# Performance work log

Hardware: AMD Instinct MI355X
Metric: run time of the kernel (lower is better)

## Reference

```python
import jax, jax.numpy as jnp
import numpy as np

B, S, D, H = 4, 2048, 1024, 16
DK = D // H

def setup_inputs() -> dict:
    key = jax.random.key(0)
    ks = jax.random.split(key, 11)
    scale = 1.0 / np.sqrt(D)
    return {
        "query": jax.random.normal(ks[0], (B, S, D), jnp.float32),
        "key_": jax.random.normal(ks[1], (B, S, D), jnp.float32),
        "value": jax.random.normal(ks[2], (B, S, D), jnp.float32),
        "Wq": jax.random.normal(ks[3], (D, D), jnp.float32) * scale,
        "bq": jnp.zeros((D,), jnp.float32),
        "Wk": jax.random.normal(ks[4], (D, D), jnp.float32) * scale,
        "bk": jnp.zeros((D,), jnp.float32),
        "Wv": jax.random.normal(ks[5], (D, D), jnp.float32) * scale,
        "bv": jnp.zeros((D,), jnp.float32),
        "Wo": jax.random.normal(ks[6], (D, D), jnp.float32) * scale,
        "bo": jnp.zeros((D,), jnp.float32),
    }

def reference(query, key_, value, Wq, bq, Wk, bk, Wv, bv, Wo, bo):
    # Linear projections (torch Linear: x @ W.T + b)
    Q = query @ Wq.T + bq            # [B,S,D]
    K = key_ @ Wk.T + bk
    V = value @ Wv.T + bv
    # split heads -> [B,H,S,DK]
    def split(x):
        return x.reshape(B, S, H, DK).transpose(0, 2, 1, 3)
    Qh, Kh, Vh = split(Q), split(K), split(V)
    scores = jnp.einsum("bhqd,bhkd->bhqk", Qh, Kh) / np.sqrt(DK)
    attn = jax.nn.softmax(scores, axis=-1)
    ctx = jnp.einsum("bhqk,bhkd->bhqd", attn, Vh)
    ctx = ctx.transpose(0, 2, 1, 3).reshape(B, S, D)
    return ctx @ Wo.T + bo
```

## Files before the change

### kernel.cpp

```cpp
#include <hip/hip_runtime.h>
#include <hip/hip_bf16.h>
#include <stdint.h>

#define B_ 4
#define S_ 2048
#define D_ 1024
#define H_ 16
#define DK_ 64
#define GM (B_ * S_)
#define GN D_
#define GK D_
#define BM 128
#define BN 128
#define BK 64
#define QBLK 128
#define KVBLK 128

typedef __attribute__((ext_vector_type(8))) __bf16 bf16x8;
typedef __attribute__((ext_vector_type(4))) float f32x4;
typedef __attribute__((ext_vector_type(4))) uint32_t u32x4;
typedef __attribute__((ext_vector_type(2))) uint32_t u32x2;

#if __has_builtin(__builtin_amdgcn_exp2f)
#define EXP2F(x) __builtin_amdgcn_exp2f(x)
#else
#define EXP2F(x) exp2f(x)
#endif

#define SCALE_LOG2E 0.18033688011112042f

__device__ __forceinline__ uint16_t f2bf(float x) {
  uint32_t u = __builtin_bit_cast(uint32_t, x);
  u += 0x7fffu + ((u >> 16) & 1u);
  return (uint16_t)(u >> 16);
}
__device__ __forceinline__ uint32_t cvtpk(float lo, float hi) {
  uint32_t r;
  asm("v_cvt_pk_bf16_f32 %0, %1, %2" : "=v"(r) : "v"(lo), "v"(hi));
  return r;
}
__device__ __forceinline__ void gload_lds16(const void* g, void* l) {
  __builtin_amdgcn_global_load_lds(
      (const __attribute__((address_space(1))) void*)g,
      (__attribute__((address_space(3))) void*)l, 16, 0, 0);
}

struct CvtArgs {
  const float* src[7];
  uint16_t* dst[7];
  int n[7];
  float scale[7];
};

__global__ __launch_bounds__(256) void cvt_f32_bf16(CvtArgs a) {
  const int z = blockIdx.z;
  const float* __restrict__ s = a.src[z];
  uint16_t* __restrict__ d = a.dst[z];
  const float sc = a.scale[z];
  const int nv = a.n[z] >> 3;
  const int stride = gridDim.x * blockDim.x;
  for (int i = blockIdx.x * blockDim.x + threadIdx.x; i < nv; i += stride) {
    f32x4 v0 = *(const f32x4*)(s + (size_t)i * 8);
    f32x4 v1 = *(const f32x4*)(s + (size_t)i * 8 + 4);
    union { uint16_t u[8]; u32x4 q; } o;
#pragma unroll
    for (int j = 0; j < 4; ++j) o.u[j] = f2bf(v0[j] * sc);
#pragma unroll
    for (int j = 0; j < 4; ++j) o.u[4 + j] = f2bf(v1[j] * sc);
    *(u32x4*)(d + (size_t)i * 8) = o.q;
  }
}

struct Gemm3Args {
  const uint16_t* A[3];
  const uint16_t* W[3];
  const float* bias[3];
  float bscale[3];
  void* C[3];
};

template <bool CF32>
__global__ __launch_bounds__(256, 2) void mha_gemm3(Gemm3Args args) {
  const int z = blockIdx.z;
  const char* __restrict__ A = (const char*)args.A[z];
  const char* __restrict__ W = (const char*)args.W[z];
  const float* __restrict__ bias = args.bias[z];
  const float bsc = args.bscale[z];
  void* __restrict__ C = args.C[z];

  __shared__ alignas(16) uint16_t tA[BM][BK];
  __shared__ alignas(16) uint16_t tW[BN][BK];

  const int tid = threadIdx.x;
  const int lane = tid & 63;
  const int wid = tid >> 6;
  const int wm = wid >> 1, wn = wid & 1;
  const int l16 = lane & 15, g = lane >> 4;

  const int m0 = blockIdx.y * BM;
  const int n0 = blockIdx.x * BN;

  f32x4 acc[4][4] = {};
  const int o = tid * 16;

  for (int k0 = 0; k0 < GK; k0 += BK) {
#pragma unroll
    for (int i = 0; i < 4; ++i) {
      const int oo = o + i * 4096;
      const int row = oo >> 7, colb = oo & 127;
      gload_lds16(A + (size_t)(m0 + row) * (GK * 2) + (size_t)k0 * 2 + colb,
                  ((char*)&tA[0][0]) + i * 4096 + wid * 1024);
      gload_lds16(W + (size_t)(n0 + row) * (GK * 2) + (size_t)k0 * 2 + colb,
                  ((char*)&tW[0][0]) + i * 4096 + wid * 1024);
    }
    __syncthreads();
#pragma unroll
    for (int kk = 0; kk < 2; ++kk) {
      const int kcol = kk * 32 + g * 8;
      bf16x8 af[4], bfr[4];
#pragma unroll
      for (int m = 0; m < 4; ++m)
        af[m] = *(const bf16x8*)&tA[wm * 64 + m * 16 + l16][kcol];
#pragma unroll
      for (int n = 0; n < 4; ++n)
        bfr[n] = *(const bf16x8*)&tW[wn * 64 + n * 16 + l16][kcol];
#pragma unroll
      for (int m = 0; m < 4; ++m)
#pragma unroll
        for (int n = 0; n < 4; ++n)
          acc[m][n] = __builtin_amdgcn_mfma_f32_16x16x32_bf16(
              af[m], bfr[n], acc[m][n], 0, 0, 0);
    }
    __syncthreads();
  }

#pragma unroll
  for (int n = 0; n < 4; ++n) {
    const int col = n0 + wn * 64 + n * 16 + l16;
    const float bv = bias[col] * bsc;
#pragma unroll
    for (int m = 0; m < 4; ++m) {
      const int rbase = m0 + wm * 64 + m * 16 + g * 4;
#pragma unroll
      for (int r = 0; r < 4; ++r) {
        const float v = acc[m][n][r] + bv;
        if (CF32)
          ((float*)C)[(size_t)(rbase + r) * GN + col] = v;
        else
          ((uint16_t*)C)[(size_t)(rbase + r) * GN + col] = f2bf(v);
      }
    }
  }
}

__global__ __launch_bounds__(256) void transpose_v(
    const uint16_t* __restrict__ Vp, uint16_t* __restrict__ Vt) {
  __shared__ alignas(16) char T[64 * 128];
  const int tid = threadIdx.x;
  const int s0 = blockIdx.x * 64;
  const int h = blockIdx.y;
  const int bb = blockIdx.z;
#pragma unroll
  for (int it = 0; it < 2; ++it) {
    const int idx = tid + it * 256;
    const int row = idx >> 3;
    const int colb = (idx & 7) * 16;
    const u32x4 v = *(const u32x4*)((const char*)Vp +
        (((size_t)bb * S_ + s0 + row) * D_ + h * DK_) * 2 + colb);
    *(u32x4*)(T + row * 128 + (colb ^ (((row >> 3) & 7) << 4))) = v;
  }
  __syncthreads();
#pragma unroll
  for (int it = 0; it < 2; ++it) {
    const int idx = tid + it * 256;
    const int dk = idx >> 3;
    const int sc = (idx & 7) * 8;
    union { uint16_t u[8]; u32x4 q; } o;
#pragma unroll
    for (int j = 0; j < 8; ++j) {
      const int row = sc + j;
      o.u[j] =
          *(const uint16_t*)(T + row * 128 + ((dk * 2) ^ (((row >> 3) & 7) << 4)));
    }
    *(u32x4*)((char*)Vt +
              (((size_t)(bb * H_ + h) * DK_ + dk) * S_ + s0 + sc) * 2) = o.q;
  }
}

__global__ __launch_bounds__(256) void mha_attn(
    const uint16_t* __restrict__ Q, const uint16_t* __restrict__ K,
    const uint16_t* __restrict__ Vt, uint16_t* __restrict__ O) {
  __shared__ alignas(16) char K_s[2][16384];
  __shared__ alignas(16) char V_s[2][16384];

  const int tid = threadIdx.x;
  const int lane = tid & 63;
  const int wid = tid >> 6;
  const int l16 = lane & 15, g = lane >> 4;

  const int d = blockIdx.x;
  const int bh = (d & 7) + ((d >> 7) << 3);
  const int qb = (d >> 3) & 15;
  const int b = bh >> 4, h = bh & 15;
  const int q0 = qb * QBLK;

  bf16x8 qf[2][2];
#pragma unroll
  for (int mi = 0; mi < 2; ++mi) {
    const uint16_t* qp = Q + ((size_t)(b * S_) + q0 + mi * 64 + wid * 16 + l16) * D_ +
                         h * DK_ + g * 8;
    qf[mi][0] = *(const bf16x8*)qp;
    qf[mi][1] = *(const bf16x8*)(qp + 32);
  }

  f32x4 o_acc[2][4] = {};
  float lpart[2] = {0.f, 0.f};

  const char* Kb = (const char*)K;
  const char* Vtb = (const char*)Vt;

  int srowK[4], scolK[4], srowV[4], scolV[4];
#pragma unroll
  for (int i = 0; i < 4; ++i) {
    const int oo = tid * 16 + i * 4096;
    srowK[i] = oo >> 7;
    scolK[i] = (oo & 127) ^ ((srowK[i] & 7) << 4);
    srowV[i] = oo >> 8;
    scolV[i] = (oo & 255) ^ ((srowV[i] & 7) << 4);
  }

#define ISSUE_LOADS(buf, kv0)                                                  \
  {                                                                            \
    _Pragma("unroll") for (int i = 0; i < 4; ++i) {                            \
      gload_lds16(Kb + (((size_t)b * S_ + (kv0) + srowK[i]) * D_ + h * DK_) * 2\
                      + scolK[i],                                              \
                  &K_s[buf][0] + i * 4096 + wid * 1024);                       \
      gload_lds16(Vtb + (((size_t)bh * DK_ + srowV[i]) * S_ + (kv0)) * 2       \
                      + scolV[i],                                              \
                  &V_s[buf][0] + i * 4096 + wid * 1024);                       \
    }                                                                          \
  }

  ISSUE_LOADS(0, 0);
  __syncthreads();
  int cur = 0;

  const int bsrc = l16 + ((g & 1) << 5);
  const int gsel = g >> 1;

  for (int kv0 = 0; kv0 < S_; kv0 += KVBLK) {
    const bool last = (kv0 + KVBLK >= S_);
    if (!last) ISSUE_LOADS(cur ^ 1, kv0 + KVBLK);

    f32x4 sacc[2][8] = {};
#pragma unroll
    for (int ks = 0; ks < 2; ++ks) {
      const int kcolb = ks * 64 + g * 16;
#pragma unroll
      for (int n = 0; n < 8; ++n) {
        const int kvr = n * 16 + l16;
        const bf16x8 kf =
            *(const bf16x8*)(&K_s[cur][0] + kvr * 128 + (kcolb ^ ((kvr & 7) << 4)));
#pragma unroll
        for (int mi = 0; mi < 2; ++mi)
          sacc[mi][n] = __builtin_amdgcn_mfma_f32_16x16x32_bf16(
              kf, qf[mi][ks], sacc[mi][n], 0, 0, 0);
      }
    }

    uint32_t pb[2][4][4];
#pragma unroll
    for (int mi = 0; mi < 2; ++mi) {
      uint32_t pk0[8][2];
#pragma unroll
      for (int n = 0; n < 8; ++n) {
        float e0 = EXP2F(sacc[mi][n][0]);
        float e1 = EXP2F(sacc[mi][n][1]);
        float e2 = EXP2F(sacc[mi][n][2]);
        float e3 = EXP2F(sacc[mi][n][3]);
        lpart[mi] += (e0 + e1) + (e2 + e3);
        pk0[n][0] = cvtpk(e0, e1);
        pk0[n][1] = cvtpk(e2, e3);
      }
#pragma unroll
      for (int ks = 0; ks < 4; ++ks)
#pragma unroll
        for (int jp = 0; jp < 4; ++jp) {
          const int srcl = bsrc + ((jp >> 1) << 4);
          const uint32_t va = __shfl(pk0[2 * ks][jp & 1], srcl, 64);
          const uint32_t vb = __shfl(pk0[2 * ks + 1][jp & 1], srcl, 64);
          pb[mi][ks][jp] = gsel ? vb : va;
        }
    }

#pragma unroll
    for (int ks = 0; ks < 4; ++ks) {
      const int kcolb = ks * 64 + g * 16;
      bf16x8 pf[2];
#pragma unroll
      for (int mi = 0; mi < 2; ++mi) {
        u32x4 t = {pb[mi][ks][0], pb[mi][ks][1], pb[mi][ks][2], pb[mi][ks][3]};
        pf[mi] = __builtin_bit_cast(bf16x8, t);
      }
#pragma unroll
      for (int n = 0; n < 4; ++n) {
        const int dkr = n * 16 + l16;
        const bf16x8 vf =
            *(const bf16x8*)(&V_s[cur][0] + dkr * 256 + (kcolb ^ ((dkr & 7) << 4)));
#pragma unroll
        for (int mi = 0; mi < 2; ++mi)
          o_acc[mi][n] = __builtin_amdgcn_mfma_f32_16x16x32_bf16(
              vf, pf[mi], o_acc[mi][n], 0, 0, 0);
      }
    }

    if (!last) __syncthreads();
    cur ^= 1;
  }

  float linv[2];
#pragma unroll
  for (int mi = 0; mi < 2; ++mi) {
    float s_ = lpart[mi];
    s_ += __shfl_xor(s_, 16, 64);
    s_ += __shfl_xor(s_, 32, 64);
    linv[mi] = 1.f / s_;
  }
#pragma unroll
  for (int mi = 0; mi < 2; ++mi) {
    const size_t row = (size_t)b * S_ + q0 + mi * 64 + wid * 16 + l16;
    uint16_t* op = O + row * D_ + h * DK_ + g * 4;
#pragma unroll
    for (int n = 0; n < 4; ++n) {
      u32x2 w;
      w[0] = cvtpk(o_acc[mi][n][0] * linv[mi], o_acc[mi][n][1] * linv[mi]);
      w[1] = cvtpk(o_acc[mi][n][2] * linv[mi], o_acc[mi][n][3] * linv[mi]);
      *(u32x2*)(op + n * 16) = w;
    }
  }
}

extern "C" void kernel_launch(void* const* d_in, const int* in_sizes, int n_in,
                              void* d_out, int out_size, void* d_ws,
                              size_t ws_size, hipStream_t stream) {
  (void)in_sizes; (void)n_in; (void)out_size; (void)ws_size;

  const float* query = (const float*)d_in[0];
  const float* key_ = (const float*)d_in[1];
  const float* value = (const float*)d_in[2];
  const float* Wq = (const float*)d_in[3];
  const float* bq = (const float*)d_in[4];
  const float* Wk = (const float*)d_in[5];
  const float* bk = (const float*)d_in[6];
  const float* Wv = (const float*)d_in[7];
  const float* bv = (const float*)d_in[8];
  const float* Wo = (const float*)d_in[9];
  const float* bo = (const float*)d_in[10];

  const size_t nact = (size_t)GM * GN;
  const size_t nw = (size_t)GN * GK;
  uint16_t* p = (uint16_t*)d_ws;
  uint16_t* qb = p; p += nact;
  uint16_t* kb = p; p += nact;
  uint16_t* vb = p; p += nact;
  uint16_t* wq = p; p += nw;
  uint16_t* wk = p; p += nw;
  uint16_t* wv = p; p += nw;
  uint16_t* wo = p; p += nw;
  uint16_t* Qp = p; p += nact;
  uint16_t* Kp = p; p += nact;
  uint16_t* Vp = p; p += nact;
  uint16_t* Cp = p; p += nact;
  uint16_t* Vt = qb;

  CvtArgs ca;
  const float* srcs[7] = {query, key_, value, Wq, Wk, Wv, Wo};
  uint16_t* dsts[7] = {qb, kb, vb, wq, wk, wv, wo};
  const int cnts[7] = {(int)nact, (int)nact, (int)nact, (int)nw,
                       (int)nw,   (int)nw,   (int)nw};
  for (int i = 0; i < 7; ++i) {
    ca.src[i] = srcs[i]; ca.dst[i] = dsts[i]; ca.n[i] = cnts[i];
    ca.scale[i] = 1.0f;
  }
  ca.scale[3] = SCALE_LOG2E;
  cvt_f32_bf16<<<dim3(512, 1, 7), dim3(256), 0, stream>>>(ca);

  Gemm3Args g1;
  g1.A[0] = qb; g1.A[1] = kb; g1.A[2] = vb;
  g1.W[0] = wq; g1.W[1] = wk; g1.W[2] = wv;
  g1.bias[0] = bq; g1.bias[1] = bk; g1.bias[2] = bv;
  g1.bscale[0] = SCALE_LOG2E; g1.bscale[1] = 1.0f; g1.bscale[2] = 1.0f;
  g1.C[0] = Qp; g1.C[1] = Kp; g1.C[2] = Vp;
  mha_gemm3<false>
      <<<dim3(GN / BN, GM / BM, 3), dim3(256), 0, stream>>>(g1);

  transpose_v<<<dim3(S_ / 64, H_, B_), dim3(256), 0, stream>>>(Vp, Vt);

  mha_attn<<<dim3((S_ / QBLK) * B_ * H_), dim3(256), 0, stream>>>(Qp, Kp, Vt, Cp);

  Gemm3Args g2;
  g2.A[0] = Cp; g2.W[0] = wo; g2.bias[0] = bo; g2.C[0] = d_out;
  g2.bscale[0] = 1.0f;
  g2.A[1] = g2.A[0]; g2.W[1] = g2.W[0]; g2.bias[1] = g2.bias[0]; g2.C[1] = g2.C[0];
  g2.bscale[1] = 1.0f;
  g2.A[2] = g2.A[0]; g2.W[2] = g2.W[0]; g2.bias[2] = g2.bias[0]; g2.C[2] = g2.C[0];
  g2.bscale[2] = 1.0f;
  mha_gemm3<true>
      <<<dim3(GN / BN, GM / BM, 1), dim3(256), 0, stream>>>(g2);
}
```

Before: 253.0 us.

## Compute V projection transposed directly, removing separate transpose kernel

The V projection is now computed as Wv @ value^T through a separate GEMM launch with a row-broadcast bias and a custom output leading dimension. This writes V already in [h*dk][b*S] layout, so the transpose_v kernel and its extra read and write of V are gone. The attention kernel's V load addressing is updated to the new layout. The fused QKV launch shrinks to two z-slices and a separate V GEMM launch is added. The transposed output stores may coalesce less well than before.

```diff
diff --git a/kernel.cpp b/kernel.cpp
--- a/kernel.cpp
+++ b/kernel.cpp
@@ -15,6 +15,7 @@
 #define BK 64
 #define QBLK 128
 #define KVBLK 128
+#define LDV 8192
 
 typedef __attribute__((ext_vector_type(8))) __bf16 bf16x8;
 typedef __attribute__((ext_vector_type(4))) float f32x4;
@@ -77,9 +78,10 @@
   const float* bias[3];
   float bscale[3];
   void* C[3];
+  int ldc[3];
 };
 
-template <bool CF32>
+template <bool CF32, bool BROW>
 __global__ __launch_bounds__(256, 2) void mha_gemm3(Gemm3Args args) {
   const int z = blockIdx.z;
   const char* __restrict__ A = (const char*)args.A[z];
@@ -87,6 +89,7 @@
   const float* __restrict__ bias = args.bias[z];
   const float bsc = args.bscale[z];
   void* __restrict__ C = args.C[z];
+  const int ldc = args.ldc[z];
 
   __shared__ alignas(16) uint16_t tA[BM][BK];
   __shared__ alignas(16) uint16_t tW[BN][BK];
@@ -137,53 +140,20 @@
 #pragma unroll
   for (int n = 0; n < 4; ++n) {
     const int col = n0 + wn * 64 + n * 16 + l16;
-    const float bv = bias[col] * bsc;
+    const float bvc = BROW ? 0.f : bias[col] * bsc;
 #pragma unroll
     for (int m = 0; m < 4; ++m) {
       const int rbase = m0 + wm * 64 + m * 16 + g * 4;
 #pragma unroll
       for (int r = 0; r < 4; ++r) {
+        const float bv = BROW ? bias[rbase + r] * bsc : bvc;
         const float v = acc[m][n][r] + bv;
         if (CF32)
-          ((float*)C)[(size_t)(rbase + r) * GN + col] = v;
+          ((float*)C)[(size_t)(rbase + r) * ldc + col] = v;
         else
-          ((uint16_t*)C)[(size_t)(rbase + r) * GN + col] = f2bf(v);
-      }
-    }
-  }
-}
-
-__global__ __launch_bounds__(256) void transpose_v(
-    const uint16_t* __restrict__ Vp, uint16_t* __restrict__ Vt) {
-  __shared__ alignas(16) char T[64 * 128];
-  const int tid = threadIdx.x;
-  const int s0 = blockIdx.x * 64;
-  const int h = blockIdx.y;
-  const int bb = blockIdx.z;
-#pragma unroll
-  for (int it = 0; it < 2; ++it) {
-    const int idx = tid + it * 256;
-    const int row = idx >> 3;
-    const int colb = (idx & 7) * 16;
-    const u32x4 v = *(const u32x4*)((const char*)Vp +
-        (((size_t)bb * S_ + s0 + row) * D_ + h * DK_) * 2 + colb);
-    *(u32x4*)(T + row * 128 + (colb ^ (((row >> 3) & 7) << 4))) = v;
-  }
-  __syncthreads();
-#pragma unroll
-  for (int it = 0; it < 2; ++it) {
-    const int idx = tid + it * 256;
-    const int dk = idx >> 3;
-    const int sc = (idx & 7) * 8;
-    union { uint16_t u[8]; u32x4 q; } o;
-#pragma unroll
-    for (int j = 0; j < 8; ++j) {
-      const int row = sc + j;
-      o.u[j] =
-          *(const uint16_t*)(T + row * 128 + ((dk * 2) ^ (((row >> 3) & 7) << 4)));
-    }
-    *(u32x4*)((char*)Vt +
-              (((size_t)(bb * H_ + h) * DK_ + dk) * S_ + s0 + sc) * 2) = o.q;
+          ((uint16_t*)C)[(size_t)(rbase + r) * ldc + col] = f2bf(v);
+      }
+    }
   }
 }
 
@@ -235,8 +205,8 @@
       gload_lds16(Kb + (((size_t)b * S_ + (kv0) + srowK[i]) * D_ + h * DK_) * 2\
                       + scolK[i],                                              \
                   &K_s[buf][0] + i * 4096 + wid * 1024);                       \
-      gload_lds16(Vtb + (((size_t)bh * DK_ + srowV[i]) * S_ + (kv0)) * 2       \
-                      + scolV[i],                                              \
+      gload_lds16(Vtb + (((size_t)h * DK_ + srowV[i]) * LDV + b * S_ + (kv0))  \
+                          * 2 + scolV[i],                                      \
                   &V_s[buf][0] + i * 4096 + wid * 1024);                       \
     }                                                                          \
   }
@@ -369,9 +339,8 @@
   uint16_t* wo = p; p += nw;
   uint16_t* Qp = p; p += nact;
   uint16_t* Kp = p; p += nact;
-  uint16_t* Vp = p; p += nact;
+  uint16_t* Vt = p; p += nact;
   uint16_t* Cp = p; p += nact;
-  uint16_t* Vt = qb;
 
   CvtArgs ca;
   const float* srcs[7] = {query, key_, value, Wq, Wk, Wv, Wo};
@@ -386,25 +355,34 @@
   cvt_f32_bf16<<<dim3(512, 1, 7), dim3(256), 0, stream>>>(ca);
 
   Gemm3Args g1;
-  g1.A[0] = qb; g1.A[1] = kb; g1.A[2] = vb;
-  g1.W[0] = wq; g1.W[1] = wk; g1.W[2] = wv;
-  g1.bias[0] = bq; g1.bias[1] = bk; g1.bias[2] = bv;
+  g1.A[0] = qb; g1.A[1] = kb; g1.A[2] = kb;
+  g1.W[0] = wq; g1.W[1] = wk; g1.W[2] = wk;
+  g1.bias[0] = bq; g1.bias[1] = bk; g1.bias[2] = bk;
   g1.bscale[0] = SCALE_LOG2E; g1.bscale[1] = 1.0f; g1.bscale[2] = 1.0f;
-  g1.C[0] = Qp; g1.C[1] = Kp; g1.C[2] = Vp;
-  mha_gemm3<false>
-      <<<dim3(GN / BN, GM / BM, 3), dim3(256), 0, stream>>>(g1);
-
-  transpose_v<<<dim3(S_ / 64, H_, B_), dim3(256), 0, stream>>>(Vp, Vt);
+  g1.C[0] = Qp; g1.C[1] = Kp; g1.C[2] = Kp;
+  g1.ldc[0] = GN; g1.ldc[1] = GN; g1.ldc[2] = GN;
+  mha_gemm3<false, false>
+      <<<dim3(GN / BN, GM / BM, 2), dim3(256), 0, stream>>>(g1);
+
+  Gemm3Args gv;
+  gv.A[0] = wv; gv.W[0] = vb; gv.bias[0] = bv; gv.bscale[0] = 1.0f;
+  gv.C[0] = Vt; gv.ldc[0] = LDV;
+  gv.A[1] = gv.A[0]; gv.W[1] = gv.W[0]; gv.bias[1] = gv.bias[0];
+  gv.bscale[1] = 1.0f; gv.C[1] = gv.C[0]; gv.ldc[1] = LDV;
+  gv.A[2] = gv.A[0]; gv.W[2] = gv.W[0]; gv.bias[2] = gv.bias[0];
+  gv.bscale[2] = 1.0f; gv.C[2] = gv.C[0]; gv.ldc[2] = LDV;
+  mha_gemm3<false, true>
+      <<<dim3(GM / BN, GK / BM, 1), dim3(256), 0, stream>>>(gv);
 
   mha_attn<<<dim3((S_ / QBLK) * B_ * H_), dim3(256), 0, stream>>>(Qp, Kp, Vt, Cp);
 
   Gemm3Args g2;
   g2.A[0] = Cp; g2.W[0] = wo; g2.bias[0] = bo; g2.C[0] = d_out;
-  g2.bscale[0] = 1.0f;
-  g2.A[1] = g2.A[0]; g2.W[1] = g2.W[0]; g2.bias[1] = g2.bias[0]; g2.C[1] = g2.C[0];
-  g2.bscale[1] = 1.0f;
-  g2.A[2] = g2.A[0]; g2.W[2] = g2.W[0]; g2.bias[2] = g2.bias[0]; g2.C[2] = g2.C[0];
-  g2.bscale[2] = 1.0f;
-  mha_gemm3<true>
+  g2.bscale[0] = 1.0f; g2.ldc[0] = GN;
+  g2.A[1] = g2.A[0]; g2.W[1] = g2.W[0]; g2.bias[1] = g2.bias[0];
+  g2.C[1] = g2.C[0]; g2.bscale[1] = 1.0f; g2.ldc[1] = GN;
+  g2.A[2] = g2.A[0]; g2.W[2] = g2.W[0]; g2.bias[2] = g2.bias[0];
+  g2.C[2] = g2.C[0]; g2.bscale[2] = 1.0f; g2.ldc[2] = GN;
+  mha_gemm3<true, false>
       <<<dim3(GN / BN, GM / BM, 1), dim3(256), 0, stream>>>(g2);
 }
```

Measured after the change: 259.7 us. +2.7%, slower.
